# Performance work log

Hardware: AMD Instinct MI355X
Metric: run time of the kernel (lower is better)

## Reference

```python
import jax, jax.numpy as jnp
import numpy as np

N_NODES = 100_000
N_EDGES = 1_600_000
D_IN = 128
D_HID = 128
D_OUT = 128
N_GRAPHS = 1024


def setup_inputs() -> dict:
    key = jax.random.key(0)
    ks = jax.random.split(key, 7)
    x = jax.random.normal(ks[0], (N_NODES, D_IN), dtype=jnp.float32)
    edge_index = jax.random.randint(ks[1], (2, N_EDGES), 0, N_NODES, dtype=jnp.int32)
    batch = jnp.sort(jax.random.randint(ks[2], (N_NODES,), 0, N_GRAPHS, dtype=jnp.int32))
    W1 = jax.random.normal(ks[3], (D_IN, D_HID), dtype=jnp.float32) * (1.0 / np.sqrt(D_IN))
    b1 = jax.random.normal(ks[4], (D_HID,), dtype=jnp.float32) * 0.01
    W2 = jax.random.normal(ks[5], (D_HID, D_OUT), dtype=jnp.float32) * (1.0 / np.sqrt(D_HID))
    b2 = jax.random.normal(ks[6], (D_OUT,), dtype=jnp.float32) * 0.01
    return {"x": x, "edge_index": edge_index, "batch": batch,
            "W1": W1, "b1": b1, "W2": W2, "b2": b2, "num_graphs": N_GRAPHS}


def gcn_conv(x, edge_index, W, b):
    """PyG GCNConv: add self-loops, symmetric deg^{-1/2} norm, linear, scatter-add."""
    n = x.shape[0]
    xw = x @ W  # [N, H] -- transform before propagate, as PyG does
    loop = jnp.arange(n, dtype=edge_index.dtype)
    src = jnp.concatenate([edge_index[0], loop])  # message source (x_j)
    dst = jnp.concatenate([edge_index[1], loop])  # aggregation target
    deg = jax.ops.segment_sum(jnp.ones_like(dst, dtype=xw.dtype), dst, num_segments=n)
    dinv = jnp.where(deg > 0, jax.lax.rsqrt(deg), 0.0)
    norm = dinv[src] * dinv[dst]  # [E+N]
    out = jax.ops.segment_sum(norm[:, None] * xw[src], dst, num_segments=n)
    return out + b


def reference(x, edge_index, batch, W1, b1, W2, b2, num_graphs):
    h = jax.nn.relu(gcn_conv(x, edge_index, W1, b1))
    h = gcn_conv(h, edge_index, W2, b2)
    # global_mean_pool over graph ids
    s = jax.ops.segment_sum(h, batch, num_segments=num_graphs)          # [G, D_OUT]
    cnt = jax.ops.segment_sum(jnp.ones((x.shape[0],), h.dtype), batch, num_segments=num_graphs)
    return s / jnp.maximum(cnt, 1.0)[:, None]
```

## Files before the change

kernel.cpp:

```cpp
#include <hip/hip_runtime.h>

constexpr int D = 128;
constexpr int PAD = 48;
constexpr int RANGES = 8;
constexpr int CHUNK = 8192;

typedef __attribute__((ext_vector_type(8))) short short8;
typedef __attribute__((ext_vector_type(4))) float floatx4;
typedef __attribute__((ext_vector_type(2))) float floatx2;
typedef unsigned short ushort_t;
typedef unsigned char uchar_t;

static inline size_t ws_align(size_t x) { return (x + 255) & ~size_t(255); }

__device__ inline unsigned pack_bf16(float a, float b) {
  unsigned ua = __float_as_uint(a), ub = __float_as_uint(b);
  ua += 0x7fffu + ((ua >> 16) & 1u);
  ub += 0x7fffu + ((ub >> 16) & 1u);
  return ((ua >> 16) & 0xffffu) | (ub & 0xffff0000u);
}
__device__ inline ushort_t f32_to_bf16u(float f) {
  unsigned u = __float_as_uint(f);
  u += 0x7fffu + ((u >> 16) & 1u);
  return (ushort_t)(u >> 16);
}
__device__ inline float bf16u_to_f32(ushort_t u) {
  return __uint_as_float(((unsigned)u) << 16);
}
__device__ inline uchar_t f32_to_fp8(float v) {
  int p = __builtin_amdgcn_cvt_pk_fp8_f32(v, v, 0, false);
  return (uchar_t)(p & 0xff);
}
__device__ inline void fp8x4_acc(unsigned u, float* v) {
  floatx2 a = __builtin_amdgcn_cvt_pk_f32_fp8((int)u, false);
  floatx2 b = __builtin_amdgcn_cvt_pk_f32_fp8((int)u, true);
  v[0] += a.x; v[1] += a.y; v[2] += b.x; v[3] += b.y;
}

__global__ __launch_bounds__(256) void k_fill_prep(
    const int* __restrict__ src, const int* __restrict__ dst,
    int* __restrict__ cnt, int* __restrict__ csrp, int E, int nodesPerRange,
    int nfill, const float* __restrict__ W1, const float* __restrict__ W2,
    ushort_t* __restrict__ w1t, ushort_t* __restrict__ w2t) {
  const int b = blockIdx.x;
  if (b >= nfill) {
    int idx = (b - nfill) * 256 + threadIdx.x;
    int k = idx >> 7, n = idx & 127;
    w1t[n * 128 + k] = f32_to_bf16u(W1[idx]);
    w2t[n * 128 + k] = f32_to_bf16u(W2[idx]);
    return;
  }
  const int r = b & (RANGES - 1);
  const int c = b / RANGES;
  const int lo = r * nodesPerRange;
  const int hi = lo + nodesPerRange;
  const int base0 = c * CHUNK;
  const int end = min(base0 + CHUNK, E);
  for (int j = base0 + threadIdx.x; j < end; j += 256) {
    int dd = dst[j];
    if (dd >= lo && dd < hi) {
      int p = atomicAdd(&cnt[dd], 1);
      if (p < PAD) csrp[dd * PAD + p] = src[j];
    }
  }
}

template <bool A_FP32>
__global__ __launch_bounds__(256) void k_gemm(
    const void* __restrict__ Av, const ushort_t* __restrict__ Wt,
    const int* __restrict__ cnt, uchar_t* __restrict__ Y, int N) {
  __shared__ ushort_t As[128 * 128];
  __shared__ ushort_t Bs[128 * 128];
  const int t = threadIdx.x;
  const int rowBase = blockIdx.x * 128;

  {
    const uint4* g = (const uint4*)Wt;
#pragma unroll
    for (int i = 0; i < 8; ++i) {
      int idx = t + 256 * i;
      int r = idx >> 4, c = idx & 15;
      int cs = c ^ (r & 15);
      *(uint4*)&Bs[r * 128 + cs * 8] = g[idx];
    }
  }
  if (A_FP32) {
    const float4* A = (const float4*)Av;
#pragma unroll
    for (int i = 0; i < 16; ++i) {
      int idx = t + 256 * i;
      int r = idx >> 5, c4 = idx & 31;
      int grow = rowBase + r;
      float4 v = make_float4(0.f, 0.f, 0.f, 0.f);
      if (grow < N) v = A[(size_t)grow * 32 + c4];
      int cs = (c4 >> 1) ^ (r & 15);
      unsigned* p = (unsigned*)&As[r * 128 + cs * 8 + (c4 & 1) * 4];
      p[0] = pack_bf16(v.x, v.y);
      p[1] = pack_bf16(v.z, v.w);
    }
  } else {
    const uint4* A = (const uint4*)Av;
#pragma unroll
    for (int i = 0; i < 8; ++i) {
      int idx = t + 256 * i;
      int r = idx >> 4, c = idx & 15;
      int grow = rowBase + r;
      uint4 v = make_uint4(0u, 0u, 0u, 0u);
      if (grow < N) v = A[(size_t)grow * 16 + c];
      int cs = c ^ (r & 15);
      *(uint4*)&As[r * 128 + cs * 8] = v;
    }
  }
  __syncthreads();

  const int w = t >> 6;
  const int l = t & 63;
  const int qd = l >> 4, lm = l & 15;
  const int mrow = w * 32;

  floatx4 acc[2][8];
#pragma unroll
  for (int i = 0; i < 2; ++i)
#pragma unroll
    for (int j = 0; j < 8; ++j) acc[i][j] = (floatx4){0.f, 0.f, 0.f, 0.f};

#pragma unroll
  for (int ks = 0; ks < 4; ++ks) {
    const int ch = ks * 4 + qd;
    const int chs = ch ^ lm;
    short8 a0 = *(const short8*)&As[(mrow + lm) * 128 + chs * 8];
    short8 a1 = *(const short8*)&As[(mrow + 16 + lm) * 128 + chs * 8];
#pragma unroll
    for (int j = 0; j < 8; ++j) {
      short8 b = *(const short8*)&Bs[(j * 16 + lm) * 128 + chs * 8];
      acc[0][j] = __builtin_amdgcn_mfma_f32_16x16x32_bf16(a0, b, acc[0][j], 0, 0, 0);
      acc[1][j] = __builtin_amdgcn_mfma_f32_16x16x32_bf16(a1, b, acc[1][j], 0, 0, 0);
    }
  }

  float s[2][4];
#pragma unroll
  for (int i = 0; i < 2; ++i)
#pragma unroll
    for (int r = 0; r < 4; ++r) {
      int grow = rowBase + mrow + i * 16 + qd * 4 + r;
      s[i][r] = (grow < N) ? rsqrtf(1.f + (float)cnt[grow]) : 0.f;
    }
#pragma unroll
  for (int i = 0; i < 2; ++i)
#pragma unroll
    for (int j = 0; j < 8; ++j)
#pragma unroll
      for (int r = 0; r < 4; ++r) {
        int grow = rowBase + mrow + i * 16 + qd * 4 + r;
        if (grow < N)
          Y[(size_t)grow * 128 + j * 16 + lm] = f32_to_fp8(s[i][r] * acc[i][j][r]);
      }
}

template <bool RELU>
__global__ __launch_bounds__(256) void k_aggregate(
    const uchar_t* __restrict__ y, const int* __restrict__ csrp,
    const int* __restrict__ cnt, const float* __restrict__ bias,
    ushort_t* __restrict__ out, int N) {
  int node = blockIdx.x * 4 + (threadIdx.x >> 6);
  if (node >= N) return;
  int l = threadIdx.x & 63;
  int eg = l >> 4, q = l & 15;
  const uint2* yb = (const uint2*)y;
  int deg0 = cnt[node];
  float dv = rsqrtf(1.f + (float)deg0);
  int deg = deg0 > PAD ? PAD : deg0;
  int idx = 0;
  if (l < PAD) idx = csrp[(size_t)node * PAD + l];
  uint2 sv = yb[(size_t)node * 16 + q];
  float vals[8] = {0.f, 0.f, 0.f, 0.f, 0.f, 0.f, 0.f, 0.f};
  const int iters = (deg + 15) >> 4;
  for (int it = 0; it < iters; ++it) {
    int p0 = it * 16 + eg;
    int p1 = p0 + 4, p2 = p0 + 8, p3 = p0 + 12;
    int s0 = __shfl(idx, p0);
    int s1 = __shfl(idx, p1);
    int s2 = __shfl(idx, p2);
    int s3 = __shfl(idx, p3);
    if (p0 < deg) {
      uint2 v = yb[(size_t)s0 * 16 + q];
      fp8x4_acc(v.x, vals); fp8x4_acc(v.y, vals + 4);
    }
    if (p1 < deg) {
      uint2 v = yb[(size_t)s1 * 16 + q];
      fp8x4_acc(v.x, vals); fp8x4_acc(v.y, vals + 4);
    }
    if (p2 < deg) {
      uint2 v = yb[(size_t)s2 * 16 + q];
      fp8x4_acc(v.x, vals); fp8x4_acc(v.y, vals + 4);
    }
    if (p3 < deg) {
      uint2 v = yb[(size_t)s3 * 16 + q];
      fp8x4_acc(v.x, vals); fp8x4_acc(v.y, vals + 4);
    }
  }
#pragma unroll
  for (int k = 0; k < 8; ++k) {
    vals[k] += __shfl_down(vals[k], 32);
    vals[k] += __shfl_down(vals[k], 16);
  }
  if (eg == 0) {
    fp8x4_acc(sv.x, vals); fp8x4_acc(sv.y, vals + 4);
    float4 b0 = ((const float4*)bias)[2 * q];
    float4 b1 = ((const float4*)bias)[2 * q + 1];
    float o[8];
    o[0] = dv * vals[0] + b0.x; o[1] = dv * vals[1] + b0.y;
    o[2] = dv * vals[2] + b0.z; o[3] = dv * vals[3] + b0.w;
    o[4] = dv * vals[4] + b1.x; o[5] = dv * vals[5] + b1.y;
    o[6] = dv * vals[6] + b1.z; o[7] = dv * vals[7] + b1.w;
    if (RELU) {
#pragma unroll
      for (int k = 0; k < 8; ++k) o[k] = fmaxf(o[k], 0.f);
    }
    uint4 pk;
    pk.x = pack_bf16(o[0], o[1]); pk.y = pack_bf16(o[2], o[3]);
    pk.z = pack_bf16(o[4], o[5]); pk.w = pack_bf16(o[6], o[7]);
    ((uint4*)out)[(size_t)node * 16 + q] = pk;
  }
}

__global__ __launch_bounds__(512) void k_pool(
    const ushort_t* __restrict__ h, const int* __restrict__ batch,
    float* __restrict__ out, int N, int G) {
  __shared__ float part[4][128];
  int g = blockIdx.x;
  int col = threadIdx.x & 127;
  int pr = threadIdx.x >> 7;
  int lo = 0, hi = N;
  while (lo < hi) { int m = (lo + hi) >> 1; if (batch[m] < g) lo = m + 1; else hi = m; }
  int start = lo;
  hi = N;
  while (lo < hi) { int m = (lo + hi) >> 1; if (batch[m] <= g) lo = m + 1; else hi = m; }
  int end = lo;
  float sum = 0.f;
  for (int r = start + pr; r < end; r += 4) sum += bf16u_to_f32(h[(size_t)r * D + col]);
  part[pr][col] = sum;
  __syncthreads();
  if (pr == 0) {
    float s = part[0][col] + part[1][col] + part[2][col] + part[3][col];
    int c = end - start;
    out[(size_t)g * D + col] = s / (float)(c > 0 ? c : 1);
  }
}

extern "C" void kernel_launch(void* const* d_in, const int* in_sizes, int n_in,
                              void* d_out, int out_size, void* d_ws, size_t ws_size,
                              hipStream_t stream) {
  const float* x  = (const float*)d_in[0];
  const int* edge = (const int*)d_in[1];
  const int* batch = (const int*)d_in[2];
  const float* W1 = (const float*)d_in[3];
  const float* b1 = (const float*)d_in[4];
  const float* W2 = (const float*)d_in[5];
  const float* b2 = (const float*)d_in[6];
  float* out = (float*)d_out;

  const int N = in_sizes[0] / D;
  const int E = in_sizes[1] / 2;
  const int G = out_size / D;
  const int* esrc = edge;
  const int* edst = edge + E;

  char* ws = (char*)d_ws;
  size_t off = 0;
  auto alloc = [&](size_t bytes) {
    char* p = ws + off;
    off = ws_align(off + bytes);
    return p;
  };
  uchar_t* bufY = (uchar_t*)alloc((size_t)N * D);
  ushort_t* bufH = (ushort_t*)alloc((size_t)N * D * 2);
  int* cnt = (int*)alloc((size_t)N * 4);
  int* csrp = (int*)alloc((size_t)N * PAD * 4);
  ushort_t* w1t = (ushort_t*)alloc((size_t)D * D * 2);
  ushort_t* w2t = (ushort_t*)alloc((size_t)D * D * 2);

  hipMemsetAsync(cnt, 0, (size_t)N * 4, stream);

  const int tb = 256;
  const int chunks = (E + CHUNK - 1) / CHUNK;
  const int nfill = chunks * RANGES;
  const int nprep = (D * D) / 256;
  const int npr = (N + RANGES - 1) / RANGES;
  k_fill_prep<<<nfill + nprep, tb, 0, stream>>>(esrc, edst, cnt, csrp, E, npr,
                                                nfill, W1, W2, w1t, w2t);

  const int gblk = (N + 127) / 128;
  k_gemm<true><<<gblk, 256, 0, stream>>>(x, w1t, cnt, bufY, N);
  k_aggregate<true><<<(N + 3) / 4, 256, 0, stream>>>(bufY, csrp, cnt, b1, bufH, N);
  k_gemm<false><<<gblk, 256, 0, stream>>>(bufH, w2t, cnt, bufY, N);
  k_aggregate<false><<<(N + 3) / 4, 256, 0, stream>>>(bufY, csrp, cnt, b2, bufH, N);
  k_pool<<<G, 512, 0, stream>>>(bufH, batch, out, N, G);
}
```

Measured before the change: 326.3 us.

## Fuse all GCN stages into one persistent cooperative kernel with grid syncs

Replaces the memset and six separate launches (fill, two GEMMs, two aggregations, pool) with one cooperative persistent kernel that moves between phases with grid.sync. The GEMM now reads A fragments straight from global memory into registers instead of staging them in shared memory, which halves LDS use and allows higher occupancy. The aim is to remove launch gaps and per-kernel tail effects. In exchange it adds grid-wide barriers, imposes a grid-stride schedule on each phase, and uses a pool loop with fewer row partitions per graph.

Result: slower. 1.145 ms (+250.8%).

```diff
diff --git a/kernel.cpp b/kernel.cpp
--- a/kernel.cpp
+++ b/kernel.cpp
@@ -1,4 +1,7 @@
 #include <hip/hip_runtime.h>
+#include <hip/hip_cooperative_groups.h>
+
+namespace cg = cooperative_groups;
 
 constexpr int D = 128;
 constexpr int PAD = 48;
@@ -37,135 +40,20 @@
   v[0] += a.x; v[1] += a.y; v[2] += b.x; v[3] += b.y;
 }
 
-__global__ __launch_bounds__(256) void k_fill_prep(
-    const int* __restrict__ src, const int* __restrict__ dst,
-    int* __restrict__ cnt, int* __restrict__ csrp, int E, int nodesPerRange,
-    int nfill, const float* __restrict__ W1, const float* __restrict__ W2,
-    ushort_t* __restrict__ w1t, ushort_t* __restrict__ w2t) {
-  const int b = blockIdx.x;
-  if (b >= nfill) {
-    int idx = (b - nfill) * 256 + threadIdx.x;
-    int k = idx >> 7, n = idx & 127;
-    w1t[n * 128 + k] = f32_to_bf16u(W1[idx]);
-    w2t[n * 128 + k] = f32_to_bf16u(W2[idx]);
-    return;
-  }
-  const int r = b & (RANGES - 1);
-  const int c = b / RANGES;
-  const int lo = r * nodesPerRange;
-  const int hi = lo + nodesPerRange;
-  const int base0 = c * CHUNK;
-  const int end = min(base0 + CHUNK, E);
-  for (int j = base0 + threadIdx.x; j < end; j += 256) {
-    int dd = dst[j];
-    if (dd >= lo && dd < hi) {
-      int p = atomicAdd(&cnt[dd], 1);
-      if (p < PAD) csrp[dd * PAD + p] = src[j];
-    }
-  }
-}
-
-template <bool A_FP32>
-__global__ __launch_bounds__(256) void k_gemm(
-    const void* __restrict__ Av, const ushort_t* __restrict__ Wt,
-    const int* __restrict__ cnt, uchar_t* __restrict__ Y, int N) {
-  __shared__ ushort_t As[128 * 128];
-  __shared__ ushort_t Bs[128 * 128];
-  const int t = threadIdx.x;
-  const int rowBase = blockIdx.x * 128;
-
-  {
-    const uint4* g = (const uint4*)Wt;
-#pragma unroll
-    for (int i = 0; i < 8; ++i) {
-      int idx = t + 256 * i;
-      int r = idx >> 4, c = idx & 15;
-      int cs = c ^ (r & 15);
-      *(uint4*)&Bs[r * 128 + cs * 8] = g[idx];
-    }
-  }
-  if (A_FP32) {
-    const float4* A = (const float4*)Av;
-#pragma unroll
-    for (int i = 0; i < 16; ++i) {
-      int idx = t + 256 * i;
-      int r = idx >> 5, c4 = idx & 31;
-      int grow = rowBase + r;
-      float4 v = make_float4(0.f, 0.f, 0.f, 0.f);
-      if (grow < N) v = A[(size_t)grow * 32 + c4];
-      int cs = (c4 >> 1) ^ (r & 15);
-      unsigned* p = (unsigned*)&As[r * 128 + cs * 8 + (c4 & 1) * 4];
-      p[0] = pack_bf16(v.x, v.y);
-      p[1] = pack_bf16(v.z, v.w);
-    }
-  } else {
-    const uint4* A = (const uint4*)Av;
-#pragma unroll
-    for (int i = 0; i < 8; ++i) {
-      int idx = t + 256 * i;
-      int r = idx >> 4, c = idx & 15;
-      int grow = rowBase + r;
-      uint4 v = make_uint4(0u, 0u, 0u, 0u);
-      if (grow < N) v = A[(size_t)grow * 16 + c];
-      int cs = c ^ (r & 15);
-      *(uint4*)&As[r * 128 + cs * 8] = v;
-    }
-  }
-  __syncthreads();
-
-  const int w = t >> 6;
-  const int l = t & 63;
-  const int qd = l >> 4, lm = l & 15;
-  const int mrow = w * 32;
-
-  floatx4 acc[2][8];
-#pragma unroll
-  for (int i = 0; i < 2; ++i)
-#pragma unroll
-    for (int j = 0; j < 8; ++j) acc[i][j] = (floatx4){0.f, 0.f, 0.f, 0.f};
-
-#pragma unroll
-  for (int ks = 0; ks < 4; ++ks) {
-    const int ch = ks * 4 + qd;
-    const int chs = ch ^ lm;
-    short8 a0 = *(const short8*)&As[(mrow + lm) * 128 + chs * 8];
-    short8 a1 = *(const short8*)&As[(mrow + 16 + lm) * 128 + chs * 8];
-#pragma unroll
-    for (int j = 0; j < 8; ++j) {
-      short8 b = *(const short8*)&Bs[(j * 16 + lm) * 128 + chs * 8];
-      acc[0][j] = __builtin_amdgcn_mfma_f32_16x16x32_bf16(a0, b, acc[0][j], 0, 0, 0);
-      acc[1][j] = __builtin_amdgcn_mfma_f32_16x16x32_bf16(a1, b, acc[1][j], 0, 0, 0);
-    }
-  }
-
-  float s[2][4];
-#pragma unroll
-  for (int i = 0; i < 2; ++i)
-#pragma unroll
-    for (int r = 0; r < 4; ++r) {
-      int grow = rowBase + mrow + i * 16 + qd * 4 + r;
-      s[i][r] = (grow < N) ? rsqrtf(1.f + (float)cnt[grow]) : 0.f;
-    }
-#pragma unroll
-  for (int i = 0; i < 2; ++i)
-#pragma unroll
-    for (int j = 0; j < 8; ++j)
-#pragma unroll
-      for (int r = 0; r < 4; ++r) {
-        int grow = rowBase + mrow + i * 16 + qd * 4 + r;
-        if (grow < N)
-          Y[(size_t)grow * 128 + j * 16 + lm] = f32_to_fp8(s[i][r] * acc[i][j][r]);
-      }
-}
-
-template <bool RELU>
-__global__ __launch_bounds__(256) void k_aggregate(
-    const uchar_t* __restrict__ y, const int* __restrict__ csrp,
-    const int* __restrict__ cnt, const float* __restrict__ bias,
-    ushort_t* __restrict__ out, int N) {
-  int node = blockIdx.x * 4 + (threadIdx.x >> 6);
-  if (node >= N) return;
-  int l = threadIdx.x & 63;
+struct MegaArgs {
+  const float* x; const int* src; const int* dst; const int* batch;
+  const float* W1; const float* b1; const float* W2; const float* b2;
+  float* out; uchar_t* bufY; ushort_t* bufH; int* cnt; int* csrp;
+  ushort_t* w1t; ushort_t* w2t;
+  int N, E, G, nfill, npr, gblk;
+};
+
+__device__ inline void agg_node(const uchar_t* __restrict__ y,
+                                const int* __restrict__ csrp,
+                                const int* __restrict__ cnt,
+                                const float* __restrict__ bias,
+                                ushort_t* __restrict__ out,
+                                int node, int l, bool relu) {
   int eg = l >> 4, q = l & 15;
   const uint2* yb = (const uint2*)y;
   int deg0 = cnt[node];
@@ -214,7 +102,7 @@
     o[2] = dv * vals[2] + b0.z; o[3] = dv * vals[3] + b0.w;
     o[4] = dv * vals[4] + b1.x; o[5] = dv * vals[5] + b1.y;
     o[6] = dv * vals[6] + b1.z; o[7] = dv * vals[7] + b1.w;
-    if (RELU) {
+    if (relu) {
 #pragma unroll
       for (int k = 0; k < 8; ++k) o[k] = fmaxf(o[k], 0.f);
     }
@@ -225,27 +113,217 @@
   }
 }
 
-__global__ __launch_bounds__(512) void k_pool(
-    const ushort_t* __restrict__ h, const int* __restrict__ batch,
-    float* __restrict__ out, int N, int G) {
-  __shared__ float part[4][128];
-  int g = blockIdx.x;
-  int col = threadIdx.x & 127;
-  int pr = threadIdx.x >> 7;
-  int lo = 0, hi = N;
-  while (lo < hi) { int m = (lo + hi) >> 1; if (batch[m] < g) lo = m + 1; else hi = m; }
-  int start = lo;
-  hi = N;
-  while (lo < hi) { int m = (lo + hi) >> 1; if (batch[m] <= g) lo = m + 1; else hi = m; }
-  int end = lo;
-  float sum = 0.f;
-  for (int r = start + pr; r < end; r += 4) sum += bf16u_to_f32(h[(size_t)r * D + col]);
-  part[pr][col] = sum;
-  __syncthreads();
-  if (pr == 0) {
-    float s = part[0][col] + part[1][col] + part[2][col] + part[3][col];
-    int c = end - start;
-    out[(size_t)g * D + col] = s / (float)(c > 0 ? c : 1);
+__global__ __launch_bounds__(256, 5) void k_mega(MegaArgs a) {
+  cg::grid_group grid = cg::this_grid();
+  __shared__ ushort_t Bs[128 * 128 / 2];
+  __shared__ ushort_t Bs2[128 * 128 / 2];
+  const int t = threadIdx.x;
+  const int b = blockIdx.x;
+  const int nb = gridDim.x;
+  const int stride = nb * 256;
+
+  auto bsw = [&](int i) -> ushort_t& { return i < 8192 ? Bs[i] : Bs2[i - 8192]; };
+
+  for (int i = b * 256 + t; i < a.N; i += stride) a.cnt[i] = 0;
+  for (int i = b * 256 + t; i < D * D; i += stride) {
+    int k = i >> 7, n = i & 127;
+    a.w1t[n * 128 + k] = f32_to_bf16u(a.W1[i]);
+    a.w2t[n * 128 + k] = f32_to_bf16u(a.W2[i]);
+  }
+  grid.sync();
+
+  for (int u = b; u < a.nfill; u += nb) {
+    const int r = u & (RANGES - 1);
+    const int c = u / RANGES;
+    const int lo = r * a.npr, hi = lo + a.npr;
+    const int base0 = c * CHUNK;
+    const int end = min(base0 + CHUNK, a.E);
+    for (int j = base0 + t; j < end; j += 256) {
+      int dd = a.dst[j];
+      if (dd >= lo && dd < hi) {
+        int p = atomicAdd(&a.cnt[dd], 1);
+        if (p < PAD) a.csrp[dd * PAD + p] = a.src[j];
+      }
+    }
+  }
+  grid.sync();
+
+  const int w = t >> 6;
+  const int l = t & 63;
+  const int qd = l >> 4, lm = l & 15;
+  const int mrow = w * 32;
+
+  {
+    const uint4* g = (const uint4*)a.w1t;
+#pragma unroll
+    for (int i = 0; i < 8; ++i) {
+      int idx = t + 256 * i;
+      int r = idx >> 4, c = idx & 15;
+      int cs = c ^ (r & 15);
+      int base = r * 128 + cs * 8;
+      uint4 v = g[idx];
+      *(uint2*)&bsw(base) = make_uint2(v.x, v.y);
+      *(uint2*)&bsw(base + 4) = make_uint2(v.z, v.w);
+    }
+    __syncthreads();
+    const floatx4* Af = (const floatx4*)a.x;
+    for (int tile = b; tile < a.gblk; tile += nb) {
+      const int rowBase = tile * 128;
+      const int row0 = rowBase + mrow + lm;
+      const int row1 = row0 + 16;
+      floatx4 acc[2][8];
+#pragma unroll
+      for (int i = 0; i < 2; ++i)
+#pragma unroll
+        for (int j = 0; j < 8; ++j) acc[i][j] = (floatx4){0.f, 0.f, 0.f, 0.f};
+#pragma unroll
+      for (int ks = 0; ks < 4; ++ks) {
+        const int ch = ks * 4 + qd;
+        floatx4 z = (floatx4){0.f, 0.f, 0.f, 0.f};
+        floatx4 v00 = z, v01 = z, v10 = z, v11 = z;
+        if (row0 < a.N) {
+          v00 = Af[(size_t)row0 * 32 + ch * 2];
+          v01 = Af[(size_t)row0 * 32 + ch * 2 + 1];
+        }
+        if (row1 < a.N) {
+          v10 = Af[(size_t)row1 * 32 + ch * 2];
+          v11 = Af[(size_t)row1 * 32 + ch * 2 + 1];
+        }
+        uint4 ua0, ua1;
+        ua0.x = pack_bf16(v00.x, v00.y); ua0.y = pack_bf16(v00.z, v00.w);
+        ua0.z = pack_bf16(v01.x, v01.y); ua0.w = pack_bf16(v01.z, v01.w);
+        ua1.x = pack_bf16(v10.x, v10.y); ua1.y = pack_bf16(v10.z, v10.w);
+        ua1.z = pack_bf16(v11.x, v11.y); ua1.w = pack_bf16(v11.z, v11.w);
+        short8 a0 = *(short8*)&ua0;
+        short8 a1 = *(short8*)&ua1;
+        const int chs = ch ^ lm;
+#pragma unroll
+        for (int j = 0; j < 8; ++j) {
+          short8 bf = *(const short8*)&bsw((j * 16 + lm) * 128 + chs * 8);
+          acc[0][j] = __builtin_amdgcn_mfma_f32_16x16x32_bf16(a0, bf, acc[0][j], 0, 0, 0);
+          acc[1][j] = __builtin_amdgcn_mfma_f32_16x16x32_bf16(a1, bf, acc[1][j], 0, 0, 0);
+        }
+      }
+      float s[2][4];
+#pragma unroll
+      for (int i = 0; i < 2; ++i)
+#pragma unroll
+        for (int r = 0; r < 4; ++r) {
+          int grow = rowBase + mrow + i * 16 + qd * 4 + r;
+          s[i][r] = (grow < a.N) ? rsqrtf(1.f + (float)a.cnt[grow]) : 0.f;
+        }
+#pragma unroll
+      for (int i = 0; i < 2; ++i)
+#pragma unroll
+        for (int j = 0; j < 8; ++j)
+#pragma unroll
+          for (int r = 0; r < 4; ++r) {
+            int grow = rowBase + mrow + i * 16 + qd * 4 + r;
+            if (grow < a.N)
+              a.bufY[(size_t)grow * 128 + j * 16 + lm] = f32_to_fp8(s[i][r] * acc[i][j][r]);
+          }
+    }
+  }
+  grid.sync();
+
+  for (int nbase = b * 4; nbase < a.N; nbase += nb * 4) {
+    int node = nbase + w;
+    if (node < a.N)
+      agg_node(a.bufY, a.csrp, a.cnt, a.b1, a.bufH, node, l, true);
+  }
+  grid.sync();
+
+  {
+    const uint4* g = (const uint4*)a.w2t;
+#pragma unroll
+    for (int i = 0; i < 8; ++i) {
+      int idx = t + 256 * i;
+      int r = idx >> 4, c = idx & 15;
+      int cs = c ^ (r & 15);
+      int base = r * 128 + cs * 8;
+      uint4 v = g[idx];
+      *(uint2*)&bsw(base) = make_uint2(v.x, v.y);
+      *(uint2*)&bsw(base + 4) = make_uint2(v.z, v.w);
+    }
+    __syncthreads();
+    const uint4* Ah = (const uint4*)a.bufH;
+    for (int tile = b; tile < a.gblk; tile += nb) {
+      const int rowBase = tile * 128;
+      const int row0 = rowBase + mrow + lm;
+      const int row1 = row0 + 16;
+      floatx4 acc[2][8];
+#pragma unroll
+      for (int i = 0; i < 2; ++i)
+#pragma unroll
+        for (int j = 0; j < 8; ++j) acc[i][j] = (floatx4){0.f, 0.f, 0.f, 0.f};
+#pragma unroll
+      for (int ks = 0; ks < 4; ++ks) {
+        const int ch = ks * 4 + qd;
+        uint4 ua0 = make_uint4(0u, 0u, 0u, 0u), ua1 = ua0;
+        if (row0 < a.N) ua0 = Ah[(size_t)row0 * 16 + ch];
+        if (row1 < a.N) ua1 = Ah[(size_t)row1 * 16 + ch];
+        short8 a0 = *(short8*)&ua0;
+        short8 a1 = *(short8*)&ua1;
+        const int chs = ch ^ lm;
+#pragma unroll
+        for (int j = 0; j < 8; ++j) {
+          short8 bf = *(const short8*)&bsw((j * 16 + lm) * 128 + chs * 8);
+          acc[0][j] = __builtin_amdgcn_mfma_f32_16x16x32_bf16(a0, bf, acc[0][j], 0, 0, 0);
+          acc[1][j] = __builtin_amdgcn_mfma_f32_16x16x32_bf16(a1, bf, acc[1][j], 0, 0, 0);
+        }
+      }
+      float s[2][4];
+#pragma unroll
+      for (int i = 0; i < 2; ++i)
+#pragma unroll
+        for (int r = 0; r < 4; ++r) {
+          int grow = rowBase + mrow + i * 16 + qd * 4 + r;
+          s[i][r] = (grow < a.N) ? rsqrtf(1.f + (float)a.cnt[grow]) : 0.f;
+        }
+#pragma unroll
+      for (int i = 0; i < 2; ++i)
+#pragma unroll
+        for (int j = 0; j < 8; ++j)
+#pragma unroll
+          for (int r = 0; r < 4; ++r) {
+            int grow = rowBase + mrow + i * 16 + qd * 4 + r;
+            if (grow < a.N)
+              a.bufY[(size_t)grow * 128 + j * 16 + lm] = f32_to_fp8(s[i][r] * acc[i][j][r]);
+          }
+    }
+  }
+  grid.sync();
+
+  for (int nbase = b * 4; nbase < a.N; nbase += nb * 4) {
+    int node = nbase + w;
+    if (node < a.N)
+      agg_node(a.bufY, a.csrp, a.cnt, a.b2, a.bufH, node, l, false);
+  }
+  grid.sync();
+
+  {
+    float* part = (float*)&Bs[0];
+    for (int g = b; g < a.G; g += nb) {
+      int col = t & 127;
+      int pr = t >> 7;
+      int lo = 0, hi = a.N;
+      while (lo < hi) { int m = (lo + hi) >> 1; if (a.batch[m] < g) lo = m + 1; else hi = m; }
+      int start = lo;
+      hi = a.N;
+      while (lo < hi) { int m = (lo + hi) >> 1; if (a.batch[m] <= g) lo = m + 1; else hi = m; }
+      int end = lo;
+      float sum = 0.f;
+      for (int r = start + pr; r < end; r += 2)
+        sum += bf16u_to_f32(a.bufH[(size_t)r * D + col]);
+      part[pr * 128 + col] = sum;
+      __syncthreads();
+      if (pr == 0) {
+        float sm = part[col] + part[128 + col];
+        int c = end - start;
+        a.out[(size_t)g * D + col] = sm / (float)(c > 0 ? c : 1);
+      }
+      __syncthreads();
+    }
   }
 }
 
@@ -264,8 +342,6 @@
   const int N = in_sizes[0] / D;
   const int E = in_sizes[1] / 2;
   const int G = out_size / D;
-  const int* esrc = edge;
-  const int* edst = edge + E;
 
   char* ws = (char*)d_ws;
   size_t off = 0;
@@ -281,20 +357,22 @@
   ushort_t* w1t = (ushort_t*)alloc((size_t)D * D * 2);
   ushort_t* w2t = (ushort_t*)alloc((size_t)D * D * 2);
 
-  hipMemsetAsync(cnt, 0, (size_t)N * 4, stream);
-
-  const int tb = 256;
+  MegaArgs a;
+  a.x = x; a.src = edge; a.dst = edge + E; a.batch = batch;
+  a.W1 = W1; a.b1 = b1; a.W2 = W2; a.b2 = b2;
+  a.out = out; a.bufY = bufY; a.bufH = bufH; a.cnt = cnt; a.csrp = csrp;
+  a.w1t = w1t; a.w2t = w2t;
+  a.N = N; a.E = E; a.G = G;
   const int chunks = (E + CHUNK - 1) / CHUNK;
-  const int nfill = chunks * RANGES;
-  const int nprep = (D * D) / 256;
-  const int npr = (N + RANGES - 1) / RANGES;
-  k_fill_prep<<<nfill + nprep, tb, 0, stream>>>(esrc, edst, cnt, csrp, E, npr,
-                                                nfill, W1, W2, w1t, w2t);
-
-  const int gblk = (N + 127) / 128;
-  k_gemm<true><<<gblk, 256, 0, stream>>>(x, w1t, cnt, bufY, N);
-  k_aggregate<true><<<(N + 3) / 4, 256, 0, stream>>>(bufY, csrp, cnt, b1, bufH, N);
-  k_gemm<false><<<gblk, 256, 0, stream>>>(bufH, w2t, cnt, bufY, N);
-  k_aggregate<false><<<(N + 3) / 4, 256, 0, stream>>>(bufY, csrp, cnt, b2, bufH, N);
-  k_pool<<<G, 512, 0, stream>>>(bufH, batch, out, N, G);
-}
+  a.nfill = chunks * RANGES;
+  a.npr = (N + RANGES - 1) / RANGES;
+  a.gblk = (N + 127) / 128;
+
+  int bpc = 0;
+  hipOccupancyMaxActiveBlocksPerMultiprocessor(&bpc, k_mega, 256, 0);
+  if (bpc < 1) bpc = 1;
+  int grid = bpc * 256;
+
+  void* kp[] = { (void*)&a };
+  hipLaunchCooperativeKernel((const void*)k_mega, dim3(grid), dim3(256), kp, 0, stream);
+}
```
